# Performance work log

Measured on AMD Instinct MI355X. Metric: run time of the kernel, lower is better.

## Reference

```python
import jax, jax.numpy as jnp
from jax import lax
import numpy as np

STRIDE = 2
EXT_PAD = (2, 2)  # computed in __init__: (total_pad - inter_pad)//2 split symmetrically


def setup_inputs() -> dict:
    key = jax.random.key(0)
    k1, k2, k3 = jax.random.split(key, 3)
    x = jax.random.normal(k1, (32, 256, 32, 32), dtype=jnp.float32)
    # Conv kernel in OIHW layout: [out_chs, in_chs, kh, kw]
    W = jax.random.normal(k2, (128, 256, 4, 4), dtype=jnp.float32) * 0.05
    b = jax.random.normal(k3, (128,), dtype=jnp.float32) * 0.01
    return {"x": x, "W": W, "b": b}


def reference(x, W, b):
    # _Interpad: insert (stride-1) zeros between every pair of adjacent spatial
    # elements (not after the last one): new_size = (size-1)*stride + 1.
    B, C, H, Wd = x.shape
    s = STRIDE
    stuffed = jnp.zeros((B, C, (H - 1) * s + 1, (Wd - 1) * s + 1), dtype=x.dtype)
    stuffed = stuffed.at[:, :, ::s, ::s].set(x)
    # external zero padding
    p = EXT_PAD
    padded = jnp.pad(stuffed, ((0, 0), (0, 0), p, p))
    # standard (cross-correlation) conv, stride 1, dilation 1, valid padding
    y = lax.conv_general_dilated(
        padded, W,
        window_strides=(1, 1),
        padding='VALID',
        rhs_dilation=(1, 1),
        dimension_numbers=('NCHW', 'OIHW', 'NCHW'),
    )
    return y + b[None, :, None, None]
```

## Files before the change

kernel.cpp:

```cpp
#include <hip/hip_runtime.h>


typedef float  f32x4  __attribute__((ext_vector_type(4)));
typedef short  short8 __attribute__((ext_vector_type(8)));
typedef unsigned short ushort4v __attribute__((ext_vector_type(4)));
typedef unsigned short ushort8v __attribute__((ext_vector_type(8)));

__device__ __forceinline__ unsigned short f2bf(float f) {
    unsigned u = __builtin_bit_cast(unsigned, f);
    u += 0x7fffu + ((u >> 16) & 1u);
    return (unsigned short)(u >> 16);
}

__device__ __forceinline__ void ld_lds16(const unsigned short* g, unsigned short* l) {
    __builtin_amdgcn_global_load_lds(
        (const __attribute__((address_space(1))) unsigned int*)g,
        (__attribute__((address_space(3))) unsigned int*)l,
        16, 0, 0);
}

#define XP_U 288
#define XP_G 9792
#define XP_N 313344
#define WP_G 8192
#define WP_PI 262144

__global__ __launch_bounds__(256) void prepack_w2(const float* __restrict__ W,
                                                  unsigned short* __restrict__ wp) {
    int t = blockIdx.x * 256 + threadIdx.x;
    int o = t >> 8, c = t & 255;
    int g = c >> 3, c8 = c & 7;
    const float4* src = (const float4*)(W + (size_t)(o * 256 + c) * 16);
    float4 q0 = src[0], q1 = src[1], q2 = src[2], q3 = src[3];
    float rows[4][4] = {{q0.x,q0.y,q0.z,q0.w},{q1.x,q1.y,q1.z,q1.w},
                        {q2.x,q2.y,q2.z,q2.w},{q3.x,q3.y,q3.z,q3.w}};
    #pragma unroll
    for (int pi = 0; pi < 2; ++pi)
    #pragma unroll
    for (int pj = 0; pj < 2; ++pj)
    #pragma unroll
    for (int du = 0; du < 2; ++du)
    #pragma unroll
    for (int dv = 0; dv < 2; ++dv)
        wp[pi*WP_PI + g*WP_G + pj*4096 + (du*2+dv)*1024 + o*8 + c8] =
            f2bf(rows[pi+2*du][pj+2*dv]);
}

__global__ __launch_bounds__(256) void prepack_x(const float* __restrict__ x,
                                                 unsigned short* __restrict__ xp) {
    __shared__ unsigned short xt[256 * 32];
    const int tid = threadIdx.x;
    const int up  = blockIdx.x;
    const int n   = blockIdx.y;
    const bool interior = (up >= 1 && up <= 32);

    if (interior) {
        const int u = up - 1;
        #pragma unroll
        for (int k = 0; k < 8; ++k) {
            int idx4 = tid + k * 256;
            int c = idx4 >> 3, v4 = idx4 & 7;
            float4 val = *(const float4*)(x + ((size_t)(n*256 + c)*32 + u)*32 + v4*4);
            ushort4v s = { f2bf(val.x), f2bf(val.y), f2bf(val.z), f2bf(val.w) };
            *(ushort4v*)&xt[c*32 + v4*4] = s;
        }
        __syncthreads();
    }

    #pragma unroll
    for (int s = 0; s < 5; ++s) {
        int id = tid + s * 256;
        if (id < 1152) {
            int g = id / 36, vp = id % 36;
            ushort8v o8 = {0,0,0,0,0,0,0,0};
            if (interior && vp >= 1 && vp <= 32) {
                #pragma unroll
                for (int e = 0; e < 8; ++e)
                    o8[e] = xt[(g*8 + e)*32 + (vp - 1)];
            }
            *(ushort8v*)&xp[(size_t)n*XP_N + g*XP_G + up*XP_U + vp*8] = o8;
        }
    }
}

__global__ __launch_bounds__(256, 4) void tconv_main(
    const unsigned short* __restrict__ xp,
    const unsigned short* __restrict__ wp,
    const float* __restrict__ bias,
    float* __restrict__ out)
{
    __shared__ __align__(16) unsigned short lds[16384];

    const int tid  = threadIdx.x;
    const int lane = tid & 63;
    const int w    = tid >> 6;
    const int pjw  = w >> 1;
    const int half = w & 1;
    const int lg   = lane >> 4;
    const int ln   = lane & 15;
    const int du   = lg >> 1, dv = lg & 1;

    const int bid = blockIdx.x;
    const int wg  = (bid & 7) * 128 + (bid >> 3);
    const int n   = wg >> 5;
    const int rem = wg & 31;
    const int aq  = rem >> 2;
    const int pi  = (rem >> 1) & 1;
    const int oh  = rem & 1;
    const int a0  = aq * 4;

    const unsigned short* xpb = xp + (size_t)n * XP_N + (a0 + pi) * XP_U
                              + ((half * 2 + du) * XP_U + (ln + pjw + dv) * 8);
    const unsigned short* wpb = wp + pi * WP_PI + oh * 512;

    const int wfoff = (pjw * 4 + lg) * 512 + ln * 8;

    f32x4 acc[4][4];
    #pragma unroll
    for (int i = 0; i < 4; ++i)
        #pragma unroll
        for (int jj = 0; jj < 4; ++jj)
            acc[i][jj] = (f32x4){0.f, 0.f, 0.f, 0.f};

    short8 xA[4], xB[4];

#define STAGE_W(P, BUF)                                                      \
    { _Pragma("unroll")                                                      \
      for (int cc_ = 0; cc_ < 2; ++cc_) {                                    \
        const unsigned short* ws_ = wpb + (size_t)(2*(P) + cc_) * WP_G;      \
        unsigned short* wd_ = (unsigned short*)lds + (BUF)*8192 + cc_*4096;  \
        _Pragma("unroll")                                                    \
        for (int s_ = 0; s_ < 2; ++s_) {                                     \
            int r_ = w * 2 + s_;                                             \
            ld_lds16(ws_ + r_ * 1024 + lane * 8,                             \
                     wd_ + r_ * 512 + lane * 8); } } }

#define LOAD_X(CH, XS)                                                      \
    { const unsigned short* xs_ = xpb + (size_t)(CH) * XP_G;                 \
      XS[0] = *(const short8*)(xs_);                                         \
      XS[1] = *(const short8*)(xs_ + 128);                                   \
      XS[2] = *(const short8*)(xs_ + XP_U);                                  \
      XS[3] = *(const short8*)(xs_ + XP_U + 128); }

#define MFMA_CHUNK(BUF, CC, XS)                                              \
    { const unsigned short* wb_ = (unsigned short*)lds + (BUF)*8192          \
                                  + (CC)*4096 + wfoff;                       \
      _Pragma("unroll")                                                      \
      for (int i_ = 0; i_ < 4; ++i_) {                                       \
          short8 av_ = *(const short8*)&wb_[i_ * 128];                       \
          _Pragma("unroll")                                                  \
          for (int jj_ = 0; jj_ < 4; ++jj_)                                  \
              acc[i_][jj_] = __builtin_amdgcn_mfma_f32_16x16x32_bf16(        \
                  av_, XS[jj_], acc[i_][jj_], 0, 0, 0);                      \
      } }

    STAGE_W(0, 0);
    __builtin_amdgcn_sched_barrier(0);
    LOAD_X(0, xA);
    LOAD_X(1, xB);
    __syncthreads();

    for (int p = 0; p < 16; ++p) {
        const int cur = p & 1;
        if (p < 15) {
            STAGE_W(p + 1, cur ^ 1);
            __builtin_amdgcn_sched_barrier(0);
        }
        MFMA_CHUNK(cur, 0, xA);
        if (p < 15) LOAD_X(2 * p + 2, xA);
        MFMA_CHUNK(cur, 1, xB);
        if (p < 15) LOAD_X(2 * p + 3, xB);
        __syncthreads();
    }

#undef MFMA_CHUNK
#undef LOAD_X
#undef STAGE_W

    float* epi = (float*)lds;
    #pragma unroll
    for (int i = 0; i < 4; ++i) {
        __syncthreads();
        f32x4 bv = *(const f32x4*)&bias[oh * 64 + i * 16 + lg * 4];
        #pragma unroll
        for (int jj = 0; jj < 4; ++jj) {
            int ar = half * 2 + (jj >> 1);
            int b  = (jj & 1) * 16 + ln;
            #pragma unroll
            for (int r = 0; r < 4; ++r)
                epi[((r * 4 + lg) * 8 + ar * 2 + pjw) * 33 + b] = acc[i][jj][r] + bv[r];
        }
        __syncthreads();
        #pragma unroll
        for (int k = 0; k < 4; ++k) {
            int f    = tid + k * 256;
            int row  = f >> 4;
            int q    = f & 15;
            float2 A = *(const float2*)&epi[(row * 2 + 0) * 33 + q * 2];
            float2 B = *(const float2*)&epi[(row * 2 + 1) * 33 + q * 2];
            float4 v = { A.x, B.x, A.y, B.y };
            int olp   = row >> 2;
            int o     = oh * 64 + i * 16 + ((olp & 3) << 2) + (olp >> 2);
            int i_out = 2 * (a0 + (row & 3)) + pi;
            *(float4*)&out[(((size_t)n * 128 + o) * 64 + i_out) * 64 + q * 4] = v;
        }
    }
}

__global__ __launch_bounds__(256) void prepack_w(const float* __restrict__ W,
                                                 unsigned short* __restrict__ Wp) {
    int t = blockIdx.x * 256 + threadIdx.x;
    int o = t >> 8, c = t & 255;
    const float4* src = (const float4*)(W + (size_t)(o * 256 + c) * 16);
    float4 q0 = src[0], q1 = src[1], q2 = src[2], q3 = src[3];
    float rows[4][4] = {{q0.x,q0.y,q0.z,q0.w},{q1.x,q1.y,q1.z,q1.w},
                        {q2.x,q2.y,q2.z,q2.w},{q3.x,q3.y,q3.z,q3.w}};
    #pragma unroll
    for (int pi = 0; pi < 2; ++pi)
    #pragma unroll
    for (int pj = 0; pj < 2; ++pj)
    #pragma unroll
    for (int du = 0; du < 2; ++du)
    #pragma unroll
    for (int dv = 0; dv < 2; ++dv)
        Wp[((((pi*2+pj)*4 + du*2+dv)*128 + o)*256) + c] = f2bf(rows[pi+2*du][pj+2*dv]);
}

template<bool PRE>
__global__ __launch_bounds__(512, 2) void tconv_mfma(
    const float* __restrict__ x, const float* __restrict__ W,
    const unsigned short* __restrict__ Wp, const float* __restrict__ bias,
    float* __restrict__ out)
{
    __shared__ __align__(16) unsigned short xsh[2][9 * 34 * 8];
    __shared__ __align__(16) unsigned short wsh[2][2 * 4 * 128 * 8];

    const int tid = threadIdx.x;
    const int bid = blockIdx.x;
    const int pi  = bid & 1;
    const int aq  = (bid >> 1) & 3;
    const int n   = bid >> 3;
    const int a0  = aq * 8;
    const int u0  = a0 + pi - 1;

    const int l   = tid & 63;
    const int w   = tid >> 6;
    const int pjw = w >> 2;
    const int q   = w & 3;
    const int lg  = l >> 4;
    const int ln  = l & 15;

    const int sv = tid & 31;
    const int sg = tid >> 5;

    f32x4 acc[8][4];
    #pragma unroll
    for (int i = 0; i < 8; ++i)
        #pragma unroll
        for (int jj = 0; jj < 4; ++jj)
            acc[i][jj] = (f32x4){0.f, 0.f, 0.f, 0.f};

    float    xv[5];
    ushort4v wv[4];
    float4   wa[2], wb[2];

    auto stage_load = [&](int ch) {
        const int c0 = ch * 8;
        #pragma unroll
        for (int s = 0; s < 5; ++s) {
            int p = sg * 5 + s;
            if (p < 72) {
                int c = p & 7, rr = p >> 3;
                int u = u0 + rr;
                xv[s] = ((unsigned)u < 32u)
                      ? x[((n*256 + c0 + c)*32 + u)*32 + sv] : 0.f;
            }
        }
        if (PRE) {
            #pragma unroll
            for (int k = 0; k < 4; ++k) {
                int uu = tid + k * 512;
                int chalf = uu & 1, o = (uu >> 1) & 127;
                int sub = (uu >> 8) & 3, pjq = (uu >> 10) & 1;
                wv[k] = *(const ushort4v*)&Wp[(((pi*2 + pjq)*4 + sub)*128 + o)*256
                                              + c0 + chalf*4];
            }
        } else {
            #pragma unroll
            for (int k = 0; k < 2; ++k) {
                int pr = tid + k * 512;
                int o = pr >> 3, c = pr & 7;
                const float* base = W + ((o*256 + c0 + c) << 4) + pi*4;
                wa[k] = *(const float4*)base;
                wb[k] = *(const float4*)(base + 8);
            }
        }
    };

    auto stage_write = [&](int buf) {
        #pragma unroll
        for (int s = 0; s < 5; ++s) {
            int p = sg * 5 + s;
            if (p < 72) {
                int c = p & 7, rr = p >> 3;
                xsh[buf][(rr*34 + sv + 1)*8 + c] = f2bf(xv[s]);
            }
        }
        if (tid < 144) {
            int pr = tid >> 1;
            int rr = pr >> 3, c = pr & 7;
            int cw = (tid & 1) * 33;
            xsh[buf][(rr*34 + cw)*8 + c] = 0;
        }
        if (PRE) {
            #pragma unroll
            for (int k = 0; k < 4; ++k) {
                int uu = tid + k * 512;
                int chalf = uu & 1, o = (uu >> 1) & 127;
                int sub = (uu >> 8) & 3, pjq = (uu >> 10) & 1;
                *(ushort4v*)&wsh[buf][(((pjq*4 + sub)*128 + o)*8) + chalf*4] = wv[k];
            }
        } else {
            #pragma unroll
            for (int k = 0; k < 2; ++k) {
                int pr = tid + k * 512;
                int o = pr >> 3, c = pr & 7;
                float ra[4] = {wa[k].x, wa[k].y, wa[k].z, wa[k].w};
                float rb[4] = {wb[k].x, wb[k].y, wb[k].z, wb[k].w};
                #pragma unroll
                for (int pj2 = 0; pj2 < 2; ++pj2)
                #pragma unroll
                for (int duu = 0; duu < 2; ++duu)
                #pragma unroll
                for (int dvv = 0; dvv < 2; ++dvv) {
                    float val = duu ? rb[pj2 + 2*dvv] : ra[pj2 + 2*dvv];
                    wsh[buf][(((pj2*4 + duu*2 + dvv)*128 + o)*8) + c] = f2bf(val);
                }
            }
        }
    };

    stage_load(0);
    stage_write(0);
    __syncthreads();

    for (int ch = 0; ch < 32; ++ch) {
        const int cur = ch & 1;
        if (ch + 1 < 32) stage_load(ch + 1);

        short8 bfr[4];
        #pragma unroll
        for (int jj = 0; jj < 4; ++jj) {
            int arow = q*2 + (jj >> 1);
            int b    = (jj & 1)*16 + ln;
            int rr   = arow + (lg >> 1);
            int cw   = b + pjw + (lg & 1);
            bfr[jj]  = *(const short8*)&xsh[cur][(rr*34 + cw)*8];
        }
        #pragma unroll
        for (int i = 0; i < 8; ++i) {
            short8 av = *(const short8*)&wsh[cur][((pjw*4 + lg)*128 + i*16 + ln)*8];
            #pragma unroll
            for (int jj = 0; jj < 4; ++jj)
                acc[i][jj] = __builtin_amdgcn_mfma_f32_16x16x32_bf16(
                                 av, bfr[jj], acc[i][jj], 0, 0, 0);
        }

        if (ch + 1 < 32) stage_write(cur ^ 1);
        __syncthreads();
    }

    #pragma unroll
    for (int i = 0; i < 8; ++i) {
        const f32x4 bv = *(const f32x4*)&bias[i*16 + lg*4];
        #pragma unroll
        for (int jj = 0; jj < 4; ++jj) {
            int arow  = q*2 + (jj >> 1);
            int b     = (jj & 1)*16 + ln;
            int i_out = 2*(a0 + arow) + pi;
            int j_out = 2*b + pjw;
            int o0    = i*16 + lg*4;
            int base  = ((n*128 + o0)*64 + i_out)*64 + j_out;
            #pragma unroll
            for (int r = 0; r < 4; ++r)
                out[base + r*4096] = acc[i][jj][r] + bv[r];
        }
    }
}

extern "C" void kernel_launch(void* const* d_in, const int* in_sizes, int n_in,
                              void* d_out, int out_size, void* d_ws, size_t ws_size,
                              hipStream_t stream) {
    const float* x    = (const float*)d_in[0];
    const float* W    = (const float*)d_in[1];
    const float* bias = (const float*)d_in[2];
    float* out        = (float*)d_out;

    const size_t wp2_bytes = (size_t)2 * WP_PI * 2;
    const size_t xp_bytes  = (size_t)32 * XP_N * 2;
    if (ws_size >= wp2_bytes + xp_bytes) {
        unsigned short* wp2 = (unsigned short*)d_ws;
        unsigned short* xpp = (unsigned short*)((char*)d_ws + wp2_bytes);
        prepack_w2<<<128, 256, 0, stream>>>(W, wp2);
        prepack_x<<<dim3(34, 32), 256, 0, stream>>>(x, xpp);
        tconv_main<<<1024, 256, 0, stream>>>(xpp, wp2, bias, out);
    } else if (ws_size >= (size_t)4*4*128*256*2) {
        unsigned short* Wp = (unsigned short*)d_ws;
        prepack_w<<<128, 256, 0, stream>>>(W, Wp);
        tconv_mfma<true><<<256, 512, 0, stream>>>(x, W, Wp, bias, out);
    } else {
        tconv_mfma<false><<<256, 512, 0, stream>>>(x, W, nullptr, bias, out);
    }
}
```

Before: 58.11 us.

## Replace full syncthreads with partial vmcnt waits, setprio around MFMAs, unroll pipeline by two

The main loop's __syncthreads, which drains every outstanding memory operation, is replaced by an explicit s_waitcnt vmcnt(8) plus s_barrier. This lets the register-prefetched X loads stay in flight across the barrier while the LDS weight stage completes. MFMA blocks are wrapped in s_setprio so waves doing compute get issue priority. The loop is also unrolled by two with a compile-time buffer index and a peeled last phase, removing the p<15 branches. The risk is that the hand-counted vmcnt value is wrong, which would allow reads of stale LDS or registers.

```diff
diff --git a/kernel.cpp b/kernel.cpp
--- a/kernel.cpp
+++ b/kernel.cpp
@@ -145,6 +145,7 @@
 #define MFMA_CHUNK(BUF, CC, XS)                                              \
     { const unsigned short* wb_ = (unsigned short*)lds + (BUF)*8192          \
                                   + (CC)*4096 + wfoff;                       \
+      __builtin_amdgcn_s_setprio(1);                                        \
       _Pragma("unroll")                                                      \
       for (int i_ = 0; i_ < 4; ++i_) {                                       \
           short8 av_ = *(const short8*)&wb_[i_ * 128];                       \
@@ -152,30 +153,47 @@
           for (int jj_ = 0; jj_ < 4; ++jj_)                                  \
               acc[i_][jj_] = __builtin_amdgcn_mfma_f32_16x16x32_bf16(        \
                   av_, XS[jj_], acc[i_][jj_], 0, 0, 0);                      \
-      } }
+      }                                                                      \
+      __builtin_amdgcn_s_setprio(0); }
+
+#define PHASE_HDR()                                                          \
+    __builtin_amdgcn_sched_barrier(0);                                       \
+    asm volatile("s_waitcnt vmcnt(8)" ::: "memory");                         \
+    __builtin_amdgcn_s_barrier();                                            \
+    __builtin_amdgcn_sched_barrier(0);
+
+#define PHASE_FULL(CUR, P)                                                   \
+    {                                                                        \
+        PHASE_HDR();                                                         \
+        STAGE_W((P) + 1, (CUR) ^ 1);                                         \
+        __builtin_amdgcn_sched_barrier(0);                                   \
+        MFMA_CHUNK(CUR, 0, xA);                                              \
+        LOAD_X(2 * (P) + 2, xA);                                             \
+        MFMA_CHUNK(CUR, 1, xB);                                              \
+        LOAD_X(2 * (P) + 3, xB);                                             \
+    }
 
     STAGE_W(0, 0);
     __builtin_amdgcn_sched_barrier(0);
     LOAD_X(0, xA);
     LOAD_X(1, xB);
-    __syncthreads();
-
-    for (int p = 0; p < 16; ++p) {
-        const int cur = p & 1;
-        if (p < 15) {
-            STAGE_W(p + 1, cur ^ 1);
-            __builtin_amdgcn_sched_barrier(0);
-        }
-        MFMA_CHUNK(cur, 0, xA);
-        if (p < 15) LOAD_X(2 * p + 2, xA);
-        MFMA_CHUNK(cur, 1, xB);
-        if (p < 15) LOAD_X(2 * p + 3, xB);
-        __syncthreads();
-    }
-
+
+    for (int pp = 0; pp < 14; pp += 2) {
+        PHASE_FULL(0, pp);
+        PHASE_FULL(1, pp + 1);
+    }
+    PHASE_FULL(0, 14);
+    PHASE_HDR();
+    MFMA_CHUNK(1, 0, xA);
+    MFMA_CHUNK(1, 1, xB);
+
+#undef PHASE_FULL
+#undef PHASE_HDR
 #undef MFMA_CHUNK
 #undef LOAD_X
 #undef STAGE_W
+
+    __syncthreads();
 
     float* epi = (float*)lds;
     #pragma unroll
```

Measured after the change: 57.79 us. No clear change (-0.6%).

## Load weights directly into registers instead of staging through LDS

Applied to the files above, without the earlier changes.

Weight fragments now go straight from global memory into registers, double-buffered alongside the activation fragments, instead of being staged into a double-buffered LDS tile with async global-to-LDS loads and per-iteration barriers. This removes the LDS round trip and the barriers in the main loop, and LDS shrinks to the epilogue buffer only. In exchange, each wave loads weight data from global memory that waves in the block used to share through LDS, which raises global/L2 traffic. Register use also grows, so the occupancy hint drops from 4 to 3 blocks per SIMD.

```diff
diff --git a/kernel.cpp b/kernel.cpp
--- a/kernel.cpp
+++ b/kernel.cpp
@@ -10,13 +10,6 @@
     unsigned u = __builtin_bit_cast(unsigned, f);
     u += 0x7fffu + ((u >> 16) & 1u);
     return (unsigned short)(u >> 16);
-}
-
-__device__ __forceinline__ void ld_lds16(const unsigned short* g, unsigned short* l) {
-    __builtin_amdgcn_global_load_lds(
-        (const __attribute__((address_space(1))) unsigned int*)g,
-        (__attribute__((address_space(3))) unsigned int*)l,
-        16, 0, 0);
 }
 
 #define XP_U 288
@@ -83,13 +76,13 @@
     }
 }
 
-__global__ __launch_bounds__(256, 4) void tconv_main(
+__global__ __launch_bounds__(256, 3) void tconv_main(
     const unsigned short* __restrict__ xp,
     const unsigned short* __restrict__ wp,
     const float* __restrict__ bias,
     float* __restrict__ out)
 {
-    __shared__ __align__(16) unsigned short lds[16384];
+    __shared__ __align__(16) float epi[4224];
 
     const int tid  = threadIdx.x;
     const int lane = tid & 63;
@@ -111,9 +104,8 @@
 
     const unsigned short* xpb = xp + (size_t)n * XP_N + (a0 + pi) * XP_U
                               + ((half * 2 + du) * XP_U + (ln + pjw + dv) * 8);
-    const unsigned short* wpb = wp + pi * WP_PI + oh * 512;
-
-    const int wfoff = (pjw * 4 + lg) * 512 + ln * 8;
+    const unsigned short* wpb = wp + pi * WP_PI + (pjw * 4 + lg) * 1024
+                              + oh * 512 + ln * 8;
 
     f32x4 acc[4][4];
     #pragma unroll
@@ -122,62 +114,46 @@
         for (int jj = 0; jj < 4; ++jj)
             acc[i][jj] = (f32x4){0.f, 0.f, 0.f, 0.f};
 
-    short8 xA[4], xB[4];
-
-#define STAGE_W(P, BUF)                                                      \
-    { _Pragma("unroll")                                                      \
-      for (int cc_ = 0; cc_ < 2; ++cc_) {                                    \
-        const unsigned short* ws_ = wpb + (size_t)(2*(P) + cc_) * WP_G;      \
-        unsigned short* wd_ = (unsigned short*)lds + (BUF)*8192 + cc_*4096;  \
-        _Pragma("unroll")                                                    \
-        for (int s_ = 0; s_ < 2; ++s_) {                                     \
-            int r_ = w * 2 + s_;                                             \
-            ld_lds16(ws_ + r_ * 1024 + lane * 8,                             \
-                     wd_ + r_ * 512 + lane * 8); } } }
-
-#define LOAD_X(CH, XS)                                                      \
+    short8 wA[4], wB[4], xA[4], xB[4];
+
+#define LOAD_W(CH, WS)                                                       \
+    { const unsigned short* ws_ = wpb + (size_t)(CH) * WP_G;                 \
+      WS[0] = *(const short8*)(ws_);                                         \
+      WS[1] = *(const short8*)(ws_ + 128);                                   \
+      WS[2] = *(const short8*)(ws_ + 256);                                   \
+      WS[3] = *(const short8*)(ws_ + 384); }
+
+#define LOAD_X(CH, XS)                                                       \
     { const unsigned short* xs_ = xpb + (size_t)(CH) * XP_G;                 \
       XS[0] = *(const short8*)(xs_);                                         \
       XS[1] = *(const short8*)(xs_ + 128);                                   \
       XS[2] = *(const short8*)(xs_ + XP_U);                                  \
       XS[3] = *(const short8*)(xs_ + XP_U + 128); }
 
-#define MFMA_CHUNK(BUF, CC, XS)                                              \
-    { const unsigned short* wb_ = (unsigned short*)lds + (BUF)*8192          \
-                                  + (CC)*4096 + wfoff;                       \
-      _Pragma("unroll")                                                      \
-      for (int i_ = 0; i_ < 4; ++i_) {                                       \
-          short8 av_ = *(const short8*)&wb_[i_ * 128];                       \
+#define MFMA16(WS, XS)                                                       \
+    { _Pragma("unroll")                                                      \
+      for (int i_ = 0; i_ < 4; ++i_)                                         \
           _Pragma("unroll")                                                  \
           for (int jj_ = 0; jj_ < 4; ++jj_)                                  \
               acc[i_][jj_] = __builtin_amdgcn_mfma_f32_16x16x32_bf16(        \
-                  av_, XS[jj_], acc[i_][jj_], 0, 0, 0);                      \
-      } }
-
-    STAGE_W(0, 0);
-    __builtin_amdgcn_sched_barrier(0);
-    LOAD_X(0, xA);
-    LOAD_X(1, xB);
-    __syncthreads();
-
-    for (int p = 0; p < 16; ++p) {
-        const int cur = p & 1;
-        if (p < 15) {
-            STAGE_W(p + 1, cur ^ 1);
-            __builtin_amdgcn_sched_barrier(0);
-        }
-        MFMA_CHUNK(cur, 0, xA);
-        if (p < 15) LOAD_X(2 * p + 2, xA);
-        MFMA_CHUNK(cur, 1, xB);
-        if (p < 15) LOAD_X(2 * p + 3, xB);
-        __syncthreads();
-    }
-
-#undef MFMA_CHUNK
+                  WS[i_], XS[jj_], acc[i_][jj_], 0, 0, 0); }
+
+    LOAD_W(0, wA); LOAD_X(0, xA);
+    LOAD_W(1, wB); LOAD_X(1, xB);
+
+    for (int ch = 0; ch < 30; ch += 2) {
+        MFMA16(wA, xA);
+        LOAD_W(ch + 2, wA); LOAD_X(ch + 2, xA);
+        MFMA16(wB, xB);
+        LOAD_W(ch + 3, wB); LOAD_X(ch + 3, xB);
+    }
+    MFMA16(wA, xA);
+    MFMA16(wB, xB);
+
+#undef MFMA16
 #undef LOAD_X
-#undef STAGE_W
-
-    float* epi = (float*)lds;
+#undef LOAD_W
+
     #pragma unroll
     for (int i = 0; i < 4; ++i) {
         __syncthreads();
```

Result: slower. 75.56 us (+30.0%).
